# Performance work log

Hardware: AMD Instinct MI355X
Metric: run time of the kernel (lower is better)

## Reference

```python
import jax, jax.numpy as jnp
import numpy as np

ALPHA, GAMMA = 0.25, 2.0
FG_W, BG_W = 13.0, 1.0
DEPTH_MIN, DEPTH_MAX, NUM_BINS = 0.001, 60.0, 80


def setup_inputs() -> dict:
    key = jax.random.key(0)
    k1, k2, k3, k4, k5, k6 = jax.random.split(key, 6)
    B, N, H, W, C = 8, 16, 96, 320, 81  # C = NUM_BINS + 1
    depth_logits = jax.random.normal(k1, (B, C, H, W), dtype=jnp.float32)
    # valid boxes: u1<u2 in [0,W], v1<v2 in [0,H]
    u1 = jax.random.uniform(k2, (B * N,)) * (W - 56)
    v1 = jax.random.uniform(k3, (B * N,)) * (H - 32)
    u2 = jnp.minimum(u1 + 8.0 + jax.random.uniform(k4, (B * N,)) * 48.0, W)
    v2 = jnp.minimum(v1 + 6.0 + jax.random.uniform(k5, (B * N,)) * 24.0, H)
    gt_boxes2d = jnp.stack([u1, v1, u2, v2], axis=-1).astype(jnp.float32)
    gt_center_depth = (1.0 + jax.random.uniform(k6, (B * N,)) * 55.0).astype(jnp.float32)
    return {
        "depth_logits": depth_logits,
        "gt_boxes2d": gt_boxes2d,
        "num_gt_per_img": N,
        "gt_center_depth": gt_center_depth,
    }


def _rasterize(gt_boxes2d, gt_center_depth, num_gt_per_img, B, H, W):
    """Vectorized box rasterization. Returns (fg_mask[B,H,W] bool, depth_maps[B,H,W]).

    Painter order in the original: boxes sorted by depth descending, later
    (smaller depth) overwrites -> final pixel depth = min depth over covering boxes.
    """
    N = num_gt_per_img
    boxes = gt_boxes2d.reshape(B, N, 4)
    u1 = jnp.floor(boxes[..., 0]).astype(jnp.int32)  # (B,N)
    v1 = jnp.floor(boxes[..., 1]).astype(jnp.int32)
    u2 = jnp.ceil(boxes[..., 2]).astype(jnp.int32)
    v2 = jnp.ceil(boxes[..., 3]).astype(jnp.int32)
    us = jnp.arange(W)
    vs = jnp.arange(H)
    cover = (
        (vs[None, None, :, None] >= v1[..., None, None])
        & (vs[None, None, :, None] < v2[..., None, None])
        & (us[None, None, None, :] >= u1[..., None, None])
        & (us[None, None, None, :] < u2[..., None, None])
    )  # (B,N,H,W) bool
    depths = gt_center_depth.reshape(B, N)
    BIG = jnp.float32(1e10)
    dmin = jnp.min(jnp.where(cover, depths[..., None, None], BIG), axis=1)  # (B,H,W)
    fg_mask = jnp.any(cover, axis=1)  # (B,H,W)
    depth_maps = jnp.where(fg_mask, dmin, jnp.float32(0.0))
    return fg_mask, depth_maps


def _bin_depths_lid(depth_map):
    """LID binning to int target indices; out-of-range/invalid -> NUM_BINS."""
    bin_size = 2.0 * (DEPTH_MAX - DEPTH_MIN) / (NUM_BINS * (1 + NUM_BINS))
    idx = -0.5 + 0.5 * jnp.sqrt(1.0 + 8.0 * (depth_map - DEPTH_MIN) / bin_size)
    invalid = (idx < 0) | (idx > NUM_BINS) | ~jnp.isfinite(idx)
    idx = jnp.where(invalid, jnp.float32(NUM_BINS), idx)
    return idx.astype(jnp.int32)  # truncation toward zero, matches .type(torch.int64) for >=0


def reference(depth_logits, gt_boxes2d, num_gt_per_img, gt_center_depth):
    B, C, H, W = depth_logits.shape
    fg_mask, depth_maps = _rasterize(gt_boxes2d, gt_center_depth, num_gt_per_img, B, H, W)
    target = _bin_depths_lid(depth_maps)  # (B,H,W) int
    # kornia-style categorical focal loss, reduction='none': -alpha*(1-p_t)^gamma*log(p_t)
    logp = jax.nn.log_softmax(depth_logits, axis=1)  # (B,C,H,W)
    logp_t = jnp.take_along_axis(logp, target[:, None, :, :], axis=1)[:, 0]  # (B,H,W)
    p_t = jnp.exp(logp_t)
    loss = -ALPHA * (1.0 - p_t) ** GAMMA * logp_t  # (B,H,W)
    # fg/bg balancer: (sum fg*w_fg*loss + sum bg*w_bg*loss) / total_pixels
    weights = jnp.where(fg_mask, jnp.float32(FG_W), jnp.float32(BG_W))
    num_pixels = jnp.float32(B * H * W)
    return jnp.sum(loss * weights) / num_pixels
```

## Files before the change

kernel.cpp:

```cpp
#include <hip/hip_runtime.h>
#include <math.h>

#define NB   8
#define NC   81
#define NH   96
#define NW   320
#define NBOX 16
#define HW   (NH * NW)
#define NPIX (NB * HW)

__global__ void ddn_zero_out(float* out) { out[0] = 0.0f; }

__global__ __launch_bounds__(256) void ddn_loss_kernel(
    const float* __restrict__ logits,
    const float* __restrict__ boxes,
    const float* __restrict__ depths,
    float* __restrict__ out)
{
    const int blocks_per_img = HW / 256;
    const int b   = blockIdx.x / blocks_per_img;
    const int pix = (blockIdx.x % blocks_per_img) * 256 + threadIdx.x;
    const int h   = pix / NW;
    const int w   = pix - h * NW;

    __shared__ float sb_u1[NBOX], sb_v1[NBOX], sb_u2[NBOX], sb_v2[NBOX], sb_d[NBOX];
    if (threadIdx.x < NBOX) {
        const int i = b * NBOX + threadIdx.x;
        sb_u1[threadIdx.x] = floorf(boxes[i * 4 + 0]);
        sb_v1[threadIdx.x] = floorf(boxes[i * 4 + 1]);
        sb_u2[threadIdx.x] = ceilf (boxes[i * 4 + 2]);
        sb_v2[threadIdx.x] = ceilf (boxes[i * 4 + 3]);
        sb_d [threadIdx.x] = depths[i];
    }
    __syncthreads();

    const float fu = (float)w, fv = (float)h;
    float dmin = 1e30f;
    bool  fg   = false;
    #pragma unroll
    for (int n = 0; n < NBOX; ++n) {
        const bool cov = (fv >= sb_v1[n]) & (fv < sb_v2[n]) &
                         (fu >= sb_u1[n]) & (fu < sb_u2[n]);
        if (cov) { fg = true; dmin = fminf(dmin, sb_d[n]); }
    }
    const float d = fg ? dmin : 0.0f;

    const float bin_size = (float)(2.0 * (60.0 - 0.001) / (80.0 * 81.0));
    const float idx = -0.5f + 0.5f * sqrtf(1.0f + 8.0f * (d - 0.001f) / bin_size);
    int tgt;
    if (!(idx >= 0.0f) || idx > 80.0f) tgt = 80;
    else                               tgt = (int)idx;

    const float* p = logits + (size_t)b * (NC * HW) + pix;
    float s  = 0.0f;
    float xt = 0.0f;
    #pragma unroll 3
    for (int c = 0; c < NC; ++c) {
        const float x = p[(size_t)c * HW];
        s += __expf(x);
        xt = (c == tgt) ? x : xt;
    }

    const float logp_t = xt - __logf(s);
    const float p_t    = __expf(logp_t);
    const float om     = 1.0f - p_t;
    const float loss   = -0.25f * om * om * logp_t;
    float v = loss * (fg ? 13.0f : 1.0f);

    #pragma unroll
    for (int off = 32; off > 0; off >>= 1) v += __shfl_down(v, off, 64);

    __shared__ float wsum[4];
    const int lane = threadIdx.x & 63;
    const int wid  = threadIdx.x >> 6;
    if (lane == 0) wsum[wid] = v;
    __syncthreads();
    if (threadIdx.x == 0) {
        const float t = wsum[0] + wsum[1] + wsum[2] + wsum[3];
        atomicAdd(out, t * (1.0f / (float)NPIX));
    }
}

extern "C" void kernel_launch(void* const* d_in, const int* in_sizes, int n_in,
                              void* d_out, int out_size, void* d_ws, size_t ws_size,
                              hipStream_t stream) {
    const float* logits = (const float*)d_in[0];
    const float* boxes  = (const float*)d_in[1];
    const float* depths = (const float*)d_in[3];
    float* out = (float*)d_out;

    ddn_zero_out<<<1, 1, 0, stream>>>(out);
    ddn_loss_kernel<<<NB * (HW / 256), 256, 0, stream>>>(logits, boxes, depths, out);
}
```

Measured before the change: 126.8 us.

## Process two pixels per thread with float2 loads and deterministic two-stage reduction

Each thread now handles two adjacent pixels, loading logits as float2 per channel, which halves the number of load instructions and shares the box vertical-coverage tests between the pair. The global atomicAdd and the zero-init kernel are replaced by per-block partials in workspace plus a single-block reduce kernel. This trades half as many blocks and threads, so less latency hiding on a memory-bound kernel, for wider loads and fewer atomics. NBLK is 480, so a 512-thread reduce covers it.

```diff
diff --git a/kernel.cpp b/kernel.cpp
--- a/kernel.cpp
+++ b/kernel.cpp
@@ -8,20 +8,27 @@
 #define NBOX 16
 #define HW   (NH * NW)
 #define NPIX (NB * HW)
+#define PPB  512
+#define NBLK (NPIX / PPB)
 
-__global__ void ddn_zero_out(float* out) { out[0] = 0.0f; }
+__device__ __forceinline__ int lid_bin(float d) {
+    const float bin_size = (float)(2.0 * (60.0 - 0.001) / (80.0 * 81.0));
+    const float idx = -0.5f + 0.5f * sqrtf(1.0f + 8.0f * (d - 0.001f) / bin_size);
+    if (!(idx >= 0.0f) || idx > 80.0f) return 80;
+    return (int)idx;
+}
 
-__global__ __launch_bounds__(256) void ddn_loss_kernel(
+__global__ __launch_bounds__(256) void ddn_main(
     const float* __restrict__ logits,
     const float* __restrict__ boxes,
     const float* __restrict__ depths,
-    float* __restrict__ out)
+    float* __restrict__ partials)
 {
-    const int blocks_per_img = HW / 256;
-    const int b   = blockIdx.x / blocks_per_img;
-    const int pix = (blockIdx.x % blocks_per_img) * 256 + threadIdx.x;
-    const int h   = pix / NW;
-    const int w   = pix - h * NW;
+    const int blocks_per_img = HW / PPB;
+    const int b    = blockIdx.x / blocks_per_img;
+    const int pix0 = (blockIdx.x % blocks_per_img) * PPB + threadIdx.x * 2;
+    const int h    = pix0 / NW;
+    const int w    = pix0 - h * NW;
 
     __shared__ float sb_u1[NBOX], sb_v1[NBOX], sb_u2[NBOX], sb_v2[NBOX], sb_d[NBOX];
     if (threadIdx.x < NBOX) {
@@ -34,38 +41,38 @@
     }
     __syncthreads();
 
-    const float fu = (float)w, fv = (float)h;
-    float dmin = 1e30f;
-    bool  fg   = false;
+    const float fv  = (float)h;
+    const float fu0 = (float)w, fu1 = (float)(w + 1);
+    float dm0 = 1e30f, dm1 = 1e30f;
+    bool  fg0 = false, fg1 = false;
     #pragma unroll
     for (int n = 0; n < NBOX; ++n) {
-        const bool cov = (fv >= sb_v1[n]) & (fv < sb_v2[n]) &
-                         (fu >= sb_u1[n]) & (fu < sb_u2[n]);
-        if (cov) { fg = true; dmin = fminf(dmin, sb_d[n]); }
+        const bool vcov = (fv >= sb_v1[n]) & (fv < sb_v2[n]);
+        const bool c0 = vcov & (fu0 >= sb_u1[n]) & (fu0 < sb_u2[n]);
+        const bool c1 = vcov & (fu1 >= sb_u1[n]) & (fu1 < sb_u2[n]);
+        if (c0) { fg0 = true; dm0 = fminf(dm0, sb_d[n]); }
+        if (c1) { fg1 = true; dm1 = fminf(dm1, sb_d[n]); }
     }
-    const float d = fg ? dmin : 0.0f;
+    const int tgt0 = lid_bin(fg0 ? dm0 : 0.0f);
+    const int tgt1 = lid_bin(fg1 ? dm1 : 0.0f);
 
-    const float bin_size = (float)(2.0 * (60.0 - 0.001) / (80.0 * 81.0));
-    const float idx = -0.5f + 0.5f * sqrtf(1.0f + 8.0f * (d - 0.001f) / bin_size);
-    int tgt;
-    if (!(idx >= 0.0f) || idx > 80.0f) tgt = 80;
-    else                               tgt = (int)idx;
-
-    const float* p = logits + (size_t)b * (NC * HW) + pix;
-    float s  = 0.0f;
-    float xt = 0.0f;
-    #pragma unroll 3
+    const float2* p = (const float2*)(logits + (size_t)b * (NC * HW) + pix0);
+    float s0 = 0.0f, s1 = 0.0f, xt0 = 0.0f, xt1 = 0.0f;
+    #pragma unroll 9
     for (int c = 0; c < NC; ++c) {
-        const float x = p[(size_t)c * HW];
-        s += __expf(x);
-        xt = (c == tgt) ? x : xt;
+        const float2 x = p[(size_t)c * (HW / 2)];
+        s0 += __expf(x.x);
+        s1 += __expf(x.y);
+        xt0 = (c == tgt0) ? x.x : xt0;
+        xt1 = (c == tgt1) ? x.y : xt1;
     }
 
-    const float logp_t = xt - __logf(s);
-    const float p_t    = __expf(logp_t);
-    const float om     = 1.0f - p_t;
-    const float loss   = -0.25f * om * om * logp_t;
-    float v = loss * (fg ? 13.0f : 1.0f);
+    const float lp0 = xt0 - __logf(s0);
+    const float lp1 = xt1 - __logf(s1);
+    const float pt0 = __expf(lp0), pt1 = __expf(lp1);
+    const float o0 = 1.0f - pt0,  o1 = 1.0f - pt1;
+    float v = (-0.25f * o0 * o0 * lp0) * (fg0 ? 13.0f : 1.0f)
+            + (-0.25f * o1 * o1 * lp1) * (fg1 ? 13.0f : 1.0f);
 
     #pragma unroll
     for (int off = 32; off > 0; off >>= 1) v += __shfl_down(v, off, 64);
@@ -75,9 +82,27 @@
     const int wid  = threadIdx.x >> 6;
     if (lane == 0) wsum[wid] = v;
     __syncthreads();
+    if (threadIdx.x == 0)
+        partials[blockIdx.x] = wsum[0] + wsum[1] + wsum[2] + wsum[3];
+}
+
+__global__ __launch_bounds__(512) void ddn_reduce(
+    const float* __restrict__ partials, float* __restrict__ out)
+{
+    float v = (threadIdx.x < NBLK) ? partials[threadIdx.x] : 0.0f;
+    #pragma unroll
+    for (int off = 32; off > 0; off >>= 1) v += __shfl_down(v, off, 64);
+
+    __shared__ float wsum[8];
+    const int lane = threadIdx.x & 63;
+    const int wid  = threadIdx.x >> 6;
+    if (lane == 0) wsum[wid] = v;
+    __syncthreads();
     if (threadIdx.x == 0) {
-        const float t = wsum[0] + wsum[1] + wsum[2] + wsum[3];
-        atomicAdd(out, t * (1.0f / (float)NPIX));
+        float t = 0.0f;
+        #pragma unroll
+        for (int i = 0; i < 8; ++i) t += wsum[i];
+        out[0] = t * (1.0f / (float)NPIX);
     }
 }
 
@@ -87,8 +112,9 @@
     const float* logits = (const float*)d_in[0];
     const float* boxes  = (const float*)d_in[1];
     const float* depths = (const float*)d_in[3];
-    float* out = (float*)d_out;
+    float* out      = (float*)d_out;
+    float* partials = (float*)d_ws;
 
-    ddn_zero_out<<<1, 1, 0, stream>>>(out);
-    ddn_loss_kernel<<<NB * (HW / 256), 256, 0, stream>>>(logits, boxes, depths, out);
+    ddn_main  <<<NBLK, 256, 0, stream>>>(logits, boxes, depths, partials);
+    ddn_reduce<<<1,    512, 0, stream>>>(partials, out);
 }
```

After: 114.0 us. -10.1%, faster.
